# Kernel optimization log

Measured on AMD Instinct MI355X. Metric: run time of the kernel, lower is better.

Reference implementation:

```python
import jax, jax.numpy as jnp
import numpy as np
from jax import lax

WINDOW_SIZE = 11
GAUSSIAN_SIGMA = 1.5
CROP_BORDER = 4
C1 = (0.01 * 255.0) ** 2
C2 = (0.03 * 255.0) ** 2


def _gaussian_kernel_window(ws: int, sigma: float) -> jnp.ndarray:
    # matches cv2.getGaussianKernel(ws, sigma) outer product
    x = jnp.arange(ws, dtype=jnp.float32) - (ws - 1) / 2.0
    g = jnp.exp(-(x ** 2) / (2.0 * sigma ** 2))
    g = g / jnp.sum(g)
    return jnp.outer(g, g)  # [ws, ws]


def _depthwise_conv(x: jnp.ndarray, kern: jnp.ndarray) -> jnp.ndarray:
    # x: [N, C, H, W]; kern: [C, 1, ws, ws]; valid padding, stride 1, groups=C
    return lax.conv_general_dilated(
        x, kern, window_strides=(1, 1), padding='VALID',
        dimension_numbers=('NCHW', 'OIHW', 'NCHW'),
        feature_group_count=x.shape[1])


def setup_inputs() -> dict:
    key = jax.random.key(0)
    k1, k2 = jax.random.split(key)
    raw_tensor = jax.random.uniform(k1, (32, 3, 512, 512), dtype=jnp.float32)
    dst_tensor = jax.random.uniform(k2, (32, 3, 512, 512), dtype=jnp.float32)
    return {"raw_tensor": raw_tensor, "dst_tensor": dst_tensor}


def reference(raw_tensor, dst_tensor):
    cb = CROP_BORDER
    raw = raw_tensor[:, :, cb:-cb, cb:-cb] * 255.0
    dst = dst_tensor[:, :, cb:-cb, cb:-cb] * 255.0
    C = raw.shape[1]
    kern = jnp.broadcast_to(
        _gaussian_kernel_window(WINDOW_SIZE, GAUSSIAN_SIGMA)[None, None],
        (C, 1, WINDOW_SIZE, WINDOW_SIZE)).astype(raw.dtype)

    raw_mean = _depthwise_conv(raw, kern)
    dst_mean = _depthwise_conv(dst, kern)
    raw_mean_sq = raw_mean ** 2
    dst_mean_sq = dst_mean ** 2
    raw_dst_mean = raw_mean * dst_mean
    raw_var = _depthwise_conv(raw * raw, kern) - raw_mean_sq
    dst_var = _depthwise_conv(dst * dst, kern) - dst_mean_sq
    raw_dst_cov = _depthwise_conv(raw * dst, kern) - raw_dst_mean

    num = (2.0 * raw_dst_mean + C1) * (2.0 * raw_dst_cov + C2)
    den = (raw_mean_sq + dst_mean_sq + C1) * (raw_var + dst_var + C2)
    ssim_map = num / den
    return jnp.mean(ssim_map, axis=(1, 2, 3)).astype(jnp.float32)  # [B]
```

## Files before the change

### kernel.cpp

```cpp
#include <hip/hip_runtime.h>


#define IMG   512
#define OUTD  494
#define CB    4
#define TW    64
#define TH    26
#define VSW   76
#define C1F   6.5025f
#define C2F   58.5225f
#define NPIX  732108.0f
#define XBLK  8
#define YBLK  19
#define SLOTS 456

#define GW(k) g[(k) <= 5 ? (k) : 10 - (k)]

__global__ __launch_bounds__(256, 4) void ssim_main(
        const float* __restrict__ raw, const float* __restrict__ dst,
        float* __restrict__ partial) {
    __shared__ float vs[4][TH][VSW];
    __shared__ float red[4];

    const int tid = threadIdx.x;
    const int bc  = blockIdx.z;
    const int b   = bc / 3;
    const int c3  = bc - b * 3;
    const int ty0 = blockIdx.y * TH;
    const int tx0 = blockIdx.x * TW;

    float g[6];
    {
        float t[6];
        #pragma unroll
        for (int k = 0; k < 6; ++k) {
            const float x = (float)(k - 5);
            t[k] = expf(-x * x * (1.0f / 4.5f));
        }
        const float s = 2.f * (t[0] + t[1] + t[2] + t[3] + t[4]) + t[5];
        const float inv = 1.0f / s;
        #pragma unroll
        for (int k = 0; k < 6; ++k) g[k] = t[k] * inv;
    }

    const float* rb = raw + (size_t)bc * (IMG * IMG);
    const float* db = dst + (size_t)bc * (IMG * IMG);

    #pragma unroll 1
    for (int t = tid; t < 494; t += 256) {
        const int rp = t / 38;
        const int xg = t - rp * 38;
        int col0 = CB + tx0 + xg * 2;
        if (col0 > IMG - 2) col0 = IMG - 2;
        const int row0 = CB + ty0 + rp * 2;

        float a0[4][2] = {{0.f}};
        float a1[4][2] = {{0.f}};
        #pragma unroll
        for (int k = 0; k < 12; ++k) {
            const int r = row0 + k;
            const float2 va = *(const float2*)(rb + (size_t)r * IMG + col0);
            const float2 vc = *(const float2*)(db + (size_t)r * IMG + col0);
            const float R[2] = {va.x, va.y};
            const float D[2] = {vc.x, vc.y};
            float s2[2], p2[2];
            #pragma unroll
            for (int c = 0; c < 2; ++c) {
                const float u = R[c] + D[c];
                s2[c] = fmaf(R[c], R[c], D[c] * D[c]);
                p2[c] = u * u;
            }
            if (k < 11) {
                const float w = GW(k);
                #pragma unroll
                for (int c = 0; c < 2; ++c) {
                    a0[0][c] = fmaf(w, R[c],  a0[0][c]);
                    a0[1][c] = fmaf(w, D[c],  a0[1][c]);
                    a0[2][c] = fmaf(w, s2[c], a0[2][c]);
                    a0[3][c] = fmaf(w, p2[c], a0[3][c]);
                }
            }
            if (k >= 1) {
                const float w = GW(k - 1);
                #pragma unroll
                for (int c = 0; c < 2; ++c) {
                    a1[0][c] = fmaf(w, R[c],  a1[0][c]);
                    a1[1][c] = fmaf(w, D[c],  a1[1][c]);
                    a1[2][c] = fmaf(w, s2[c], a1[2][c]);
                    a1[3][c] = fmaf(w, p2[c], a1[3][c]);
                }
            }
        }
        #pragma unroll
        for (int f = 0; f < 4; ++f) {
            *(float2*)&vs[f][rp * 2 + 0][xg * 2] = make_float2(a0[f][0], a0[f][1]);
            *(float2*)&vs[f][rp * 2 + 1][xg * 2] = make_float2(a1[f][0], a1[f][1]);
        }
    }
    __syncthreads();

    const int row = tid & 31;
    const int xg  = tid >> 5;
    const int ox0 = tx0 + xg * 8;

    #define HCONV(f, o)                                                      \
    {                                                                        \
        const float4* vp = (const float4*)&vs[f][row][xg * 8];               \
        const float4 A = vp[0], B = vp[1], Cq = vp[2], Dq = vp[3];           \
        const float2 E2 = *(const float2*)&vs[f][row][xg * 8 + 16];          \
        const float w_[18] = {A.x, A.y, A.z, A.w,  B.x, B.y, B.z, B.w,       \
                              Cq.x, Cq.y, Cq.z, Cq.w, Dq.x, Dq.y, Dq.z, Dq.w,\
                              E2.x, E2.y};                                   \
        _Pragma("unroll")                                                    \
        for (int c = 0; c < 8; ++c) {                                        \
            float t5 = g[5] * w_[c + 5];                                     \
            _Pragma("unroll")                                                \
            for (int j = 0; j < 5; ++j)                                      \
                t5 = fmaf(g[j], w_[c + j] + w_[c + 10 - j], t5);             \
            o[c] = t5;                                                       \
        }                                                                    \
    }

    float ssum = 0.f;
    if (row < TH) {
        float m0[8], m1[8];
        HCONV(0, m0);
        HCONV(1, m1);
        float q1[8], q2[8];
        #pragma unroll
        for (int c = 0; c < 8; ++c) {
            const float a = m0[c] * 255.0f;
            const float d = m1[c] * 255.0f;
            q1[c] = fmaf(a, a, d * d);
            q2[c] = a * d;
        }
        float S2[8];
        HCONV(2, S2);
        float den[8];
        #pragma unroll
        for (int c = 0; c < 8; ++c) {
            S2[c] *= 65025.0f;
            den[c] = (q1[c] + C1F) * ((S2[c] - q1[c]) + C2F);
        }
        float P2[8];
        HCONV(3, P2);
        #pragma unroll
        for (int c = 0; c < 8; ++c) {
            if (ox0 + c < OUTD) {
                const float P   = P2[c] * 65025.0f;
                const float num = fmaf(2.0f, q2[c], C1F) *
                                  ((P - S2[c]) - 2.0f * q2[c] + C2F);
                ssum = fmaf(num, __builtin_amdgcn_rcpf(den[c]), ssum);
            }
        }
    }

    #pragma unroll
    for (int off = 32; off > 0; off >>= 1)
        ssum += __shfl_down(ssum, off, 64);
    const int lane = tid & 63, wv = tid >> 6;
    if (lane == 0) red[wv] = ssum;
    __syncthreads();
    if (tid == 0) {
        const float t = red[0] + red[1] + red[2] + red[3];
        partial[(size_t)b * SLOTS + (blockIdx.y * gridDim.x + blockIdx.x) * 3 + c3] = t;
    }
}

__global__ __launch_bounds__(128) void ssim_final(
        const float* __restrict__ partial, float* __restrict__ out) {
    __shared__ float red[2];
    const int b = blockIdx.x, tid = threadIdx.x;
    float s = 0.f;
    for (int i = tid; i < SLOTS; i += 128) s += partial[(size_t)b * SLOTS + i];
    #pragma unroll
    for (int off = 32; off > 0; off >>= 1) s += __shfl_down(s, off, 64);
    if ((tid & 63) == 0) red[tid >> 6] = s;
    __syncthreads();
    if (tid == 0) out[b] = (red[0] + red[1]) * (1.0f / NPIX);
}

extern "C" void kernel_launch(void* const* d_in, const int* in_sizes, int n_in,
                              void* d_out, int out_size, void* d_ws, size_t ws_size,
                              hipStream_t stream) {
    const float* raw = (const float*)d_in[0];
    const float* dst = (const float*)d_in[1];
    float* out     = (float*)d_out;
    float* partial = (float*)d_ws;

    dim3 grid(XBLK, YBLK, 96);
    ssim_main<<<grid, 256, 0, stream>>>(raw, dst, partial);
    ssim_final<<<32, 128, 0, stream>>>(partial, out);
}
```

Baseline: 279.0 us.

## Compute nine vertical outputs per thread in vertical conv pass to cut redundant loads

Result: faster. 238.2 us (-14.6%).

```diff
diff --git a/kernel.cpp b/kernel.cpp
--- a/kernel.cpp
+++ b/kernel.cpp
@@ -13,6 +13,7 @@
 #define XBLK  8
 #define YBLK  19
 #define SLOTS 456
+#define NV    9
 
 #define GW(k) g[(k) <= 5 ? (k) : 10 - (k)]
 
@@ -46,56 +47,47 @@
     const float* rb = raw + (size_t)bc * (IMG * IMG);
     const float* db = dst + (size_t)bc * (IMG * IMG);
 
-    #pragma unroll 1
-    for (int t = tid; t < 494; t += 256) {
-        const int rp = t / 38;
-        const int xg = t - rp * 38;
-        int col0 = CB + tx0 + xg * 2;
-        if (col0 > IMG - 2) col0 = IMG - 2;
-        const int row0 = CB + ty0 + rp * 2;
+    if (tid < 228) {
+        const int c  = tid % 76;
+        const int rg = tid / 76;
+        const int start = (rg == 2) ? 17 : rg * 9;
+        int gcol = CB + tx0 + c;
+        if (gcol > IMG - 1) gcol = IMG - 1;
+        const int row0 = CB + ty0 + start;
 
-        float a0[4][2] = {{0.f}};
-        float a1[4][2] = {{0.f}};
+        const float* rp_ = rb + (size_t)row0 * IMG + gcol;
+        const float* dp_ = db + (size_t)row0 * IMG + gcol;
+
+        float acc[4][NV];
         #pragma unroll
-        for (int k = 0; k < 12; ++k) {
-            const int r = row0 + k;
-            const float2 va = *(const float2*)(rb + (size_t)r * IMG + col0);
-            const float2 vc = *(const float2*)(db + (size_t)r * IMG + col0);
-            const float R[2] = {va.x, va.y};
-            const float D[2] = {vc.x, vc.y};
-            float s2[2], p2[2];
+        for (int f = 0; f < 4; ++f)
             #pragma unroll
-            for (int c = 0; c < 2; ++c) {
-                const float u = R[c] + D[c];
-                s2[c] = fmaf(R[c], R[c], D[c] * D[c]);
-                p2[c] = u * u;
-            }
-            if (k < 11) {
-                const float w = GW(k);
-                #pragma unroll
-                for (int c = 0; c < 2; ++c) {
-                    a0[0][c] = fmaf(w, R[c],  a0[0][c]);
-                    a0[1][c] = fmaf(w, D[c],  a0[1][c]);
-                    a0[2][c] = fmaf(w, s2[c], a0[2][c]);
-                    a0[3][c] = fmaf(w, p2[c], a0[3][c]);
-                }
-            }
-            if (k >= 1) {
-                const float w = GW(k - 1);
-                #pragma unroll
-                for (int c = 0; c < 2; ++c) {
-                    a1[0][c] = fmaf(w, R[c],  a1[0][c]);
-                    a1[1][c] = fmaf(w, D[c],  a1[1][c]);
-                    a1[2][c] = fmaf(w, s2[c], a1[2][c]);
-                    a1[3][c] = fmaf(w, p2[c], a1[3][c]);
+            for (int o = 0; o < NV; ++o) acc[f][o] = 0.f;
+
+        #pragma unroll
+        for (int k = 0; k < NV + 10; ++k) {
+            const float R = rp_[(size_t)k * IMG];
+            const float D = dp_[(size_t)k * IMG];
+            const float u  = R + D;
+            const float s2 = fmaf(R, R, D * D);
+            const float p2 = u * u;
+            #pragma unroll
+            for (int o = 0; o < NV; ++o) {
+                const int kk = k - o;
+                if (kk >= 0 && kk <= 10) {
+                    const float w = GW(kk);
+                    acc[0][o] = fmaf(w, R,  acc[0][o]);
+                    acc[1][o] = fmaf(w, D,  acc[1][o]);
+                    acc[2][o] = fmaf(w, s2, acc[2][o]);
+                    acc[3][o] = fmaf(w, p2, acc[3][o]);
                 }
             }
         }
         #pragma unroll
-        for (int f = 0; f < 4; ++f) {
-            *(float2*)&vs[f][rp * 2 + 0][xg * 2] = make_float2(a0[f][0], a0[f][1]);
-            *(float2*)&vs[f][rp * 2 + 1][xg * 2] = make_float2(a1[f][0], a1[f][1]);
-        }
+        for (int f = 0; f < 4; ++f)
+            #pragma unroll
+            for (int o = 0; o < NV; ++o)
+                vs[f][start + o][c] = acc[f][o];
     }
     __syncthreads();
 
```
